# Optimization experiments

Hardware: AMD Instinct MI355X
Metric: run time of the kernel (lower is better)

The kernel has to match this reference:

```python
import jax, jax.numpy as jnp
import numpy as np

N = 9            # n
MIN_D, MAX_D = 4, 9        # 2**l, 3**l with l=2
MIN_SPLIT, MAX_SPLIT = 2, 3  # 2**(l-1), 3**(l-1)
N_SPAN = 2       # 3**(l-1) - 2**(l-1) + 1
STRIDE = N_SPAN


def _combos():
    kk0, pairs = {}, {}
    for length in range(MIN_D, MAX_D + 1):
        kk = np.arange(MIN_SPLIT, length - MIN_SPLIT + 1)
        kk = kk[(kk <= MAX_SPLIT) & (kk >= length - MAX_SPLIT)]
        kk0[length] = kk.tolist()
        p = [(k1, k2)
             for k1 in range(MIN_SPLIT, length - MIN_SPLIT + 1)
             for k2 in range(k1 + 1, length)]
        p = [(k1, k2) for (k1, k2) in p
             if k1 <= MAX_SPLIT
             and MIN_SPLIT <= k2 - k1 <= MAX_SPLIT
             and MIN_SPLIT <= length - k2 <= MAX_SPLIT]
        pairs[length] = p
    return kk0, pairs

KK0, PAIRS = _combos()


def setup_inputs() -> dict:
    key = jax.random.key(0)
    k1, k2, k3, k4 = jax.random.split(key, 4)
    B, CIN, COUT, LIN = 16384, 128, 128, 18
    return {
        "x": jax.random.normal(k1, (B, CIN, LIN), jnp.float32),
        "sum_of_squares": jax.random.normal(k2, (B,), jnp.float32),
        "filter_2": jax.random.normal(k3, (COUT, CIN, 2), jnp.float32),
        "filter_3": jax.random.normal(k4, (COUT, CIN, 3), jnp.float32),
    }


def _forward(x, filter_2, filter_3):
    # x: [B, C, 18]. Each (length, split) combo is a strided conv whose filter
    # has only 2 or 3 nonzero taps; we gather exactly those taps and contract.
    B, C, _ = x.shape
    O = filter_2.shape[0]
    s2 = 1.0 / np.sqrt(C * 2.0)
    s3 = 1.0 / np.sqrt(C * 3.0)
    outs = []
    for length in range(MIN_D, MAX_D + 1):
        T = N - length + 1  # output positions for this length
        base = np.arange(T) * STRIDE  # [T] start offsets of the strided conv
        out_d = jnp.zeros((B, O, T), x.dtype)
        kks = KK0[length]
        if kks:
            # nonzero tap positions of the zero-padded filter_2 copies
            pos = np.array([[kk - MIN_SPLIT, kk + length - MIN_SPLIT]
                            for kk in kks])           # [M, 2]
            idx = base[None, :, None] + pos[:, None, :]  # [M, T, 2]
            xg = x[:, :, idx]                            # [B, C, M, T, 2]
            out_d = out_d + jnp.einsum('bcmtk,ock->bot', xg, filter_2) * s2
        prs = PAIRS[length]
        if prs:
            pos = np.array([[k1 - MIN_SPLIT, k1 + k2 - MIN_SPLIT, k2 + length - MIN_SPLIT]
                            for (k1, k2) in prs])      # [M, 3]
            idx = base[None, :, None] + pos[:, None, :]  # [M, T, 3]
            xg = x[:, :, idx]                            # [B, C, M, T, 3]
            out_d = out_d + jnp.einsum('bcmtk,ock->bot', xg, filter_3) * s3
        out_d = jnp.pad(out_d, ((0, 0), (0, 0), (0, N - T)))  # pad to n=9
        outs.append(out_d)
    inter = jnp.stack(outs, axis=3)        # [B, O, N, max_d-min_d+1]
    return inter.reshape(B, O, -1)         # interleaved: [B, O, 54]


def reference(x, sum_of_squares, filter_2, filter_3):
    return (_forward(x, filter_2, filter_3), sum_of_squares)
```

## Files before the change

kernel.cpp:

```cpp
#include <hip/hip_runtime.h>
#include <hip/hip_bf16.h>


using short8 = short __attribute__((ext_vector_type(8)));
using f32x4  = float __attribute__((ext_vector_type(4)));

#define DEVINL __device__ __forceinline__

DEVINL unsigned short f2bf(float f) {
    unsigned int u = __float_as_uint(f);
    unsigned int r = u + 0x7FFFu + ((u >> 16) & 1u);
    return (unsigned short)(r >> 16);
}

__constant__ constexpr int START[16] = {0,6,12,18,23,31,37,46,54,63,69,77,82,88,94,100};
__constant__ constexpr int SLOT[100] = {
 0,1,2,3,3,4,
 1,2,3,4,4,5,
 6,7,8,9,9,10,
 7,8,9,10,10,
 0,11,12,13,2,14,14,3,
 12,1,13,14,3,4,
 15,6,16,1,17,8,9,3,4,
 16,7,17,2,9,10,4,5,
 18,11,19,7,13,2,14,9,10,
 19,12,8,14,3,10,
 20,15,12,17,8,14,3,3,
 16,13,9,4,4,
 18,16,13,9,9,4,
 19,17,14,10,10,5,
 20,19,17,14,14,10
};
__constant__ constexpr int JJ[100] = {
 0,0,2,2,2,2,
 0,0,2,2,2,2,
 0,0,2,2,2,2,
 0,0,2,2,2,
 1,0,0,2,3,2,2,3,
 0,1,0,2,3,3,
 0,1,0,1,2,3,3,3,3,
 0,1,0,1,3,3,3,3,
 0,1,0,1,3,4,3,3,3,
 0,1,1,3,4,3,
 0,1,1,3,4,3,4,4,
 1,1,4,4,4,
 1,1,4,4,4,4,
 1,1,4,4,4,4,
 1,1,4,4,4,4
};
__constant__ constexpr int UCOL[21] = {0,1,2,3,4,5,6,7,8,9,10,12,13,14,15,18,19,20,24,25,30};

__global__ __launch_bounds__(256)
void pack_filters(const float* __restrict__ f2, const float* __restrict__ f3,
                  unsigned short* __restrict__ bp)
{
    int p = blockIdx.x * 256 + threadIdx.x;
    if (p >= 10240) return;
    int L   = p & 63;
    int t   = p >> 6;
    int q   = t & 3;
    int j   = (t >> 2) % 5;
    int wid = t / 20;
    int o   = wid * 16 + (L & 15);
    int c0  = q * 32 + (L >> 4) * 8;
    float scale = (j < 2) ? 0.0625f : 0.051031036307982884f;
    unsigned short v[8];
    #pragma unroll
    for (int e = 0; e < 8; ++e) {
        int c = c0 + e;
        float f = (j < 2) ? f2[(o * 128 + c) * 2 + j]
                          : f3[(o * 128 + c) * 3 + (j - 2)];
        v[e] = f2bf(f * scale);
    }
    *reinterpret_cast<short8*>(bp + (long)p * 8) = *reinterpret_cast<const short8*>(v);
}

__global__ __launch_bounds__(512, 2)
void conv1d_ell_kernel(const float* __restrict__ x,
                       const unsigned short* __restrict__ bpack,
                       float* __restrict__ out)
{
    __shared__ __align__(16) unsigned char smem[89088];
    unsigned short* xl = reinterpret_cast<unsigned short*>(smem);
    float*          ob = reinterpret_cast<float*>(smem + 61440);

    const int tid  = threadIdx.x;
    const int lane = tid & 63;
    const int wid  = tid >> 6;
    const int m    = lane & 15;
    const int kblk = lane >> 4;
    const int g    = lane >> 4;

    const long b_base = (long)blockIdx.x * 16;

    #pragma unroll
    for (int q = 0; q < 4; ++q) {
        int r = tid + q * 512;
        int b = r >> 7;
        int c = r & 127;
        const float* px = x + (b_base + b) * 2304 + (long)c * 18;
        float v[16];
        #pragma unroll
        for (int t = 0; t < 8; ++t) {
            float2 w = reinterpret_cast<const float2*>(px)[t];
            v[2*t] = w.x; v[2*t+1] = w.y;
        }
        #pragma unroll
        for (int i = 0; i < 15; ++i) {
            int idx = (i * 2048 + b * 128 + c) ^ ((b & 7) << 3);
            xl[idx] = f2bf(v[i]);
        }
    }

    short8 bfrag[5][4];
    {
        const unsigned short* bp = bpack + ((long)(wid * 20) * 64 + lane) * 8;
        #pragma unroll
        for (int j = 0; j < 5; ++j)
            #pragma unroll
            for (int q = 0; q < 4; ++q)
                bfrag[j][q] = *reinterpret_cast<const short8*>(bp + (long)(j * 4 + q) * 64 * 8);
    }

    f32x4 acc[21];
    #pragma unroll
    for (int s = 0; s < 21; ++s) acc[s] = (f32x4){0.f, 0.f, 0.f, 0.f};

    __syncthreads();

    #pragma unroll
    for (int i = 0; i < 15; ++i) {
        short8 a[4];
        #pragma unroll
        for (int q = 0; q < 4; ++q) {
            int c0 = q * 32 + kblk * 8;
            int idx = (i * 2048 + m * 128 + c0) ^ ((m & 7) << 3);
            a[q] = *reinterpret_cast<const short8*>(&xl[idx]);
        }
        #pragma unroll
        for (int n = START[i]; n < START[i + 1]; ++n) {
            const int s = SLOT[n];
            const int j = JJ[n];
            #pragma unroll
            for (int q = 0; q < 4; ++q) {
                acc[s] = __builtin_amdgcn_mfma_f32_16x16x32_bf16(a[q], bfrag[j][q], acc[s], 0, 0, 0);
            }
        }
    }

    float* wbuf = ob + wid * 864;

    {
        float4 z = make_float4(0.f, 0.f, 0.f, 0.f);
        #pragma unroll
        for (int t = 0; t < 3; ++t)
            *reinterpret_cast<float4*>(wbuf + 4 * (lane + 64 * t)) = z;
        if (lane < 24)
            *reinterpret_cast<float4*>(wbuf + 4 * (lane + 192)) = z;
    }

    #pragma unroll
    for (int k = 0; k < 16; ++k) {
        if (g == (k >> 2)) {
            float* dst = wbuf + m * 54;
            #pragma unroll
            for (int s = 0; s < 21; ++s) dst[UCOL[s]] = acc[s][k & 3];
        }
        asm volatile("s_waitcnt lgkmcnt(0)" ::: "memory");
        float* dstg = out + ((b_base + k) * 128 + wid * 16) * 54;
        #pragma unroll
        for (int t = 0; t < 3; ++t) {
            float4 w = *reinterpret_cast<const float4*>(wbuf + 4 * (lane + 64 * t));
            *reinterpret_cast<float4*>(dstg + 4 * (lane + 64 * t)) = w;
        }
        if (lane < 24) {
            float4 w = *reinterpret_cast<const float4*>(wbuf + 4 * (lane + 192));
            *reinterpret_cast<float4*>(dstg + 4 * (lane + 192)) = w;
        }
    }
}

extern "C" void kernel_launch(void* const* d_in, const int* in_sizes, int n_in,
                              void* d_out, int out_size, void* d_ws, size_t ws_size,
                              hipStream_t stream) {
    const float* x   = (const float*)d_in[0];
    const float* sos = (const float*)d_in[1];
    const float* f2  = (const float*)d_in[2];
    const float* f3  = (const float*)d_in[3];
    float* out = (float*)d_out;
    unsigned short* bp = (unsigned short*)d_ws;

    pack_filters<<<dim3(40), dim3(256), 0, stream>>>(f2, f3, bp);
    conv1d_ell_kernel<<<dim3(1024), dim3(512), 0, stream>>>(x, bp, out);

    (void)hipMemcpyAsync(out + 113246208LL, sos, 16384 * sizeof(float),
                         hipMemcpyDeviceToDevice, stream);
}
```

Before: 141.8 us.

## Process two batch tiles per block and prefetch next tile during output writes

Each block now handles 32 batch rows in two 16-row passes, halving the grid. Global loads for the second tile's x are issued while the first tile's results are written out, and the converted bf16 data is stored to LDS inside that loop, so load latency overlaps with output stores. This also amortizes the per-block filter fragment loads over twice the work. The cost is fewer blocks (512 on a large GPU), which lowers parallelism, and more register pressure from the in-flight prefetch buffer.

```diff
diff --git a/kernel.cpp b/kernel.cpp
--- a/kernel.cpp
+++ b/kernel.cpp
@@ -91,7 +91,7 @@
     const int kblk = lane >> 4;
     const int g    = lane >> 4;
 
-    const long b_base = (long)blockIdx.x * 16;
+    const long b_base = (long)blockIdx.x * 32;
 
     #pragma unroll
     for (int q = 0; q < 4; ++q) {
@@ -126,30 +126,33 @@
     #pragma unroll
     for (int s = 0; s < 21; ++s) acc[s] = (f32x4){0.f, 0.f, 0.f, 0.f};
 
+    auto compute = [&]() {
+        #pragma unroll
+        for (int i = 0; i < 15; ++i) {
+            short8 a[4];
+            #pragma unroll
+            for (int q = 0; q < 4; ++q) {
+                int c0 = q * 32 + kblk * 8;
+                int idx = (i * 2048 + m * 128 + c0) ^ ((m & 7) << 3);
+                a[q] = *reinterpret_cast<const short8*>(&xl[idx]);
+            }
+            #pragma unroll
+            for (int n = START[i]; n < START[i + 1]; ++n) {
+                const int s = SLOT[n];
+                const int j = JJ[n];
+                #pragma unroll
+                for (int q = 0; q < 4; ++q) {
+                    acc[s] = __builtin_amdgcn_mfma_f32_16x16x32_bf16(a[q], bfrag[j][q], acc[s], 0, 0, 0);
+                }
+            }
+        }
+    };
+
     __syncthreads();
-
-    #pragma unroll
-    for (int i = 0; i < 15; ++i) {
-        short8 a[4];
-        #pragma unroll
-        for (int q = 0; q < 4; ++q) {
-            int c0 = q * 32 + kblk * 8;
-            int idx = (i * 2048 + m * 128 + c0) ^ ((m & 7) << 3);
-            a[q] = *reinterpret_cast<const short8*>(&xl[idx]);
-        }
-        #pragma unroll
-        for (int n = START[i]; n < START[i + 1]; ++n) {
-            const int s = SLOT[n];
-            const int j = JJ[n];
-            #pragma unroll
-            for (int q = 0; q < 4; ++q) {
-                acc[s] = __builtin_amdgcn_mfma_f32_16x16x32_bf16(a[q], bfrag[j][q], acc[s], 0, 0, 0);
-            }
-        }
-    }
+    compute();
+    __syncthreads();
 
     float* wbuf = ob + wid * 864;
-
     {
         float4 z = make_float4(0.f, 0.f, 0.f, 0.f);
         #pragma unroll
@@ -159,6 +162,54 @@
             *reinterpret_cast<float4*>(wbuf + 4 * (lane + 192)) = z;
     }
 
+    float2 pend[8];
+    #pragma unroll
+    for (int k = 0; k < 16; ++k) {
+        if ((k & 3) == 0) {
+            const int q = k >> 2;
+            const int r = tid + q * 512;
+            const int b = r >> 7, c = r & 127;
+            const float* px = x + (b_base + 16 + b) * 2304 + (long)c * 18;
+            #pragma unroll
+            for (int t = 0; t < 8; ++t)
+                pend[t] = reinterpret_cast<const float2*>(px)[t];
+        }
+        if ((k & 3) == 2) {
+            const int q = k >> 2;
+            const int r = tid + q * 512;
+            const int b = r >> 7, c = r & 127;
+            #pragma unroll
+            for (int t = 0; t < 8; ++t) {
+                const int i0 = 2 * t;
+                xl[(i0 * 2048 + b * 128 + c) ^ ((b & 7) << 3)] = f2bf(pend[t].x);
+                if (i0 + 1 < 15)
+                    xl[((i0 + 1) * 2048 + b * 128 + c) ^ ((b & 7) << 3)] = f2bf(pend[t].y);
+            }
+        }
+        if (g == (k >> 2)) {
+            float* dst = wbuf + m * 54;
+            #pragma unroll
+            for (int s = 0; s < 21; ++s) dst[UCOL[s]] = acc[s][k & 3];
+        }
+        asm volatile("s_waitcnt lgkmcnt(0)" ::: "memory");
+        float* dstg = out + ((b_base + k) * 128 + wid * 16) * 54;
+        #pragma unroll
+        for (int t = 0; t < 3; ++t) {
+            float4 w = *reinterpret_cast<const float4*>(wbuf + 4 * (lane + 64 * t));
+            *reinterpret_cast<float4*>(dstg + 4 * (lane + 64 * t)) = w;
+        }
+        if (lane < 24) {
+            float4 w = *reinterpret_cast<const float4*>(wbuf + 4 * (lane + 192));
+            *reinterpret_cast<float4*>(dstg + 4 * (lane + 192)) = w;
+        }
+    }
+
+    __syncthreads();
+
+    #pragma unroll
+    for (int s = 0; s < 21; ++s) acc[s] = (f32x4){0.f, 0.f, 0.f, 0.f};
+    compute();
+
     #pragma unroll
     for (int k = 0; k < 16; ++k) {
         if (g == (k >> 2)) {
@@ -167,7 +218,7 @@
             for (int s = 0; s < 21; ++s) dst[UCOL[s]] = acc[s][k & 3];
         }
         asm volatile("s_waitcnt lgkmcnt(0)" ::: "memory");
-        float* dstg = out + ((b_base + k) * 128 + wid * 16) * 54;
+        float* dstg = out + ((b_base + 16 + k) * 128 + wid * 16) * 54;
         #pragma unroll
         for (int t = 0; t < 3; ++t) {
             float4 w = *reinterpret_cast<const float4*>(wbuf + 4 * (lane + 64 * t));
@@ -191,7 +242,7 @@
     unsigned short* bp = (unsigned short*)d_ws;
 
     pack_filters<<<dim3(40), dim3(256), 0, stream>>>(f2, f3, bp);
-    conv1d_ell_kernel<<<dim3(1024), dim3(512), 0, stream>>>(x, bp, out);
+    conv1d_ell_kernel<<<dim3(512), dim3(512), 0, stream>>>(x, bp, out);
 
     (void)hipMemcpyAsync(out + 113246208LL, sos, 16384 * sizeof(float),
                          hipMemcpyDeviceToDevice, stream);
```

Result: slower. 154.4 us (+8.9%).
